# Kernel tuning notes

Hardware: AMD Instinct MI355X
Metric: run time of the kernel (lower is better)

The kernel has to match this reference:

```python
import jax, jax.numpy as jnp
import numpy as np
from jax import lax


def conv2d(x, w, pad):
    return lax.conv_general_dilated(x, w, (1, 1), [(pad, pad), (pad, pad)],
                                    dimension_numbers=('NCHW', 'OIHW', 'NCHW'))


def deform_conv2d(x, offset, w, b, k, pad):
    # torchvision-style DeformConv2d, stride 1, dilation 1, 1 group.
    # offset: [B, 2*k*k, H, W], pairs ordered (dy, dx) per kernel tap (row-major).
    B, C, H, W = x.shape
    KK = k * k
    off = offset.reshape(B, KK, 2, H, W)
    ky, kx = jnp.meshgrid(jnp.arange(k), jnp.arange(k), indexing='ij')
    ky = ky.reshape(1, KK, 1, 1).astype(x.dtype)
    kx = kx.reshape(1, KK, 1, 1).astype(x.dtype)
    gy = jnp.arange(H, dtype=x.dtype).reshape(1, 1, H, 1)
    gx = jnp.arange(W, dtype=x.dtype).reshape(1, 1, 1, W)
    ys = gy + ky - pad + off[:, :, 0]  # [B, KK, H, W]
    xs = gx + kx - pad + off[:, :, 1]
    y0 = jnp.floor(ys)
    x0 = jnp.floor(xs)
    y1 = y0 + 1.0
    x1 = x0 + 1.0
    img = x.reshape(B, C, H * W)

    def corner(yc, xc, wt):
        # zero padding outside the image
        valid = (yc >= 0) & (yc <= H - 1) & (xc >= 0) & (xc <= W - 1)
        idx = (jnp.clip(yc, 0, H - 1) * W + jnp.clip(xc, 0, W - 1)).astype(jnp.int32).reshape(B, -1)
        g = jax.vmap(lambda im, ix: jnp.take(im, ix, axis=1))(img, idx)  # [B, C, KK*H*W]
        return g.reshape(B, C, KK, H, W) * (wt * valid)[:, None]

    v = (corner(y0, x0, (y1 - ys) * (x1 - xs))
         + corner(y0, x1, (y1 - ys) * (xs - x0))
         + corner(y1, x0, (ys - y0) * (x1 - xs))
         + corner(y1, x1, (ys - y0) * (xs - x0)))  # [B, C, KK, H, W]
    out = jnp.einsum('bckhw,ock->bohw', v, w.reshape(w.shape[0], C, KK))
    return out + b[None, :, None, None]


def setup_inputs() -> dict:
    key = jax.random.key(0)
    ks = jax.random.split(key, 16)
    f32 = jnp.float32
    dim = 64

    def rn(k, shape, s):
        return jax.random.normal(k, shape, f32) * s

    return {
        'x': rn(ks[0], (4, dim, 96, 96), 1.0),
        'w_off3': rn(ks[1], (18, dim, 3, 3), 0.01), 'b_off3': jnp.zeros((18,), f32),
        'w_off5': rn(ks[2], (50, dim, 3, 3), 0.01), 'b_off5': jnp.zeros((50,), f32),
        'w_off7': rn(ks[3], (98, dim, 3, 3), 0.01), 'b_off7': jnp.zeros((98,), f32),
        'w_d3': rn(ks[4], (dim, dim, 3, 3), 0.04), 'b_d3': rn(ks[5], (dim,), 0.01),
        'w_d5': rn(ks[6], (dim, dim, 5, 5), 0.025), 'b_d5': rn(ks[7], (dim,), 0.01),
        'w_d7': rn(ks[8], (dim, dim, 7, 7), 0.018), 'b_d7': rn(ks[9], (dim,), 0.01),
        'w_sp': rn(ks[10], (1, 2, 7, 7), 0.1),
        'w_ca1': rn(ks[11], (12, 3 * dim, 1, 1), 0.07),
        'w_ca2': rn(ks[12], (3 * dim, 12, 1, 1), 0.28),
    }


def reference(x, w_off3, b_off3, w_off5, b_off5, w_off7, b_off7,
              w_d3, b_d3, w_d5, b_d5, w_d7, b_d7, w_sp, w_ca1, w_ca2):
    off3 = conv2d(x, w_off3, 1) + b_off3[None, :, None, None]
    off5 = conv2d(x, w_off5, 1) + b_off5[None, :, None, None]
    off7 = conv2d(x, w_off7, 1) + b_off7[None, :, None, None]
    a1 = deform_conv2d(x, off3, w_d3, b_d3, 3, 1)
    a2 = deform_conv2d(x, off5, w_d5, b_d5, 5, 2)
    a3 = deform_conv2d(x, off7, w_d7, b_d7, 7, 3)
    res = jnp.concatenate([a1, a2, a3], axis=1)  # [B, 3C, H, W]

    # SpatialAttention: channel mean/max -> 7x7 conv -> sigmoid
    sp_in = jnp.concatenate([jnp.mean(res, axis=1, keepdims=True),
                             jnp.max(res, axis=1, keepdims=True)], axis=1)
    sp = jax.nn.sigmoid(conv2d(sp_in, w_sp, 3))  # [B, 1, H, W]

    # ChannelAttention: shared MLP on avg- and max-pooled descriptors
    def fc(t):
        return conv2d(jnp.maximum(conv2d(t, w_ca1, 0), 0.0), w_ca2, 0)

    avg = jnp.mean(res, axis=(2, 3), keepdims=True)
    mx = jnp.max(res, axis=(2, 3), keepdims=True)
    ch = jax.nn.sigmoid(fc(avg) + fc(mx))  # [B, 3C, 1, 1]

    C = x.shape[1]
    c1, c2, c3 = ch[:, :C], ch[:, C:2 * C], ch[:, 2 * C:]
    return a1 * (sp + c1) + a2 * (sp + c2) + a3 * (sp + c3)
```

## Files before the change

kernel.cpp:

```cpp
#include <hip/hip_runtime.h>
#include <math.h>

#define H 96
#define W 96
#define HW (H*W)
#define CIN 64
#define NB 4
#define NOFF 166
#define OFFROW 168

typedef __attribute__((ext_vector_type(8)))  short short8;
typedef __attribute__((ext_vector_type(8)))  _Float16 half8;
typedef __attribute__((ext_vector_type(16))) float f32x16;
typedef unsigned short ushort_t;

static const size_t OFF_ALL = 0;
static const size_t RES     = OFF_ALL + (size_t)NB*HW*OFFROW;
static const size_t XB16    = RES + (size_t)NB*192*HW;
static const size_t WTD3    = XB16 + (size_t)NB*64*HW/2;
static const size_t WTD5    = WTD3 + 9*4096/2;
static const size_t WTD7    = WTD5 + 25*4096/2;
static const size_t WOFF    = WTD7 + 49*4096/2;
static const size_t BOFF    = WOFF + 9*192*64/2;
static const size_t SPIN    = BOFF + 192;
static const size_t SPATT   = SPIN + (size_t)NB*2*HW;
static const size_t POOLAVG = SPATT + (size_t)NB*HW;
static const size_t POOLMAX = POOLAVG + NB*192;
static const size_t CHATT   = POOLMAX + NB*192;

__device__ __forceinline__ ushort_t f2h(float f) {
    _Float16 h = (_Float16)f;
    return __builtin_bit_cast(unsigned short, h);
}
__device__ __forceinline__ half8 as_h8(short8 s) {
    return __builtin_bit_cast(half8, s);
}
__device__ __forceinline__ half8 splat8(float f) {
    _Float16 h = (_Float16)f;
    half8 v;
    #pragma unroll
    for (int j = 0; j < 8; j++) v[j] = h;
    return v;
}

__global__ __launch_bounds__(256) void convert_x_nhwc_kernel(const float* __restrict__ x,
                                                             ushort_t* __restrict__ xb) {
    __shared__ ushort_t tile[64][66];
    int t = threadIdx.x;
    int b = blockIdx.x / 144;
    int p0 = (blockIdx.x % 144) * 64;
    int q = t >> 6, ln = t & 63;
    #pragma unroll
    for (int i = 0; i < 16; i++) {
        int c = q * 16 + i;
        tile[ln][c] = f2h(x[((size_t)(b * 64 + c)) * HW + p0 + ln]);
    }
    __syncthreads();
    #pragma unroll
    for (int i = 0; i < 16; i++) {
        int pos = q * 16 + i;
        xb[((size_t)b * HW + p0 + pos) * 64 + ln] = tile[pos][ln];
    }
}

__global__ void convert_wt_all_kernel(const float* __restrict__ w3, const float* __restrict__ w5,
                                      const float* __restrict__ w7,
                                      ushort_t* __restrict__ wt3, ushort_t* __restrict__ wt5,
                                      ushort_t* __restrict__ wt7) {
    int idx = blockIdx.x * 256 + threadIdx.x;
    const float* src; ushort_t* dst; int KK; int o;
    if (idx < 9 * 4096)       { src = w3; dst = wt3; KK = 9;  o = idx; }
    else if (idx < 34 * 4096) { src = w5; dst = wt5; KK = 25; o = idx - 9 * 4096; }
    else if (idx < 83 * 4096) { src = w7; dst = wt7; KK = 49; o = idx - 34 * 4096; }
    else return;
    int j    = o & 7;
    int l31  = (o >> 3) & 31;
    int lh   = (o >> 8) & 1;
    int cs   = (o >> 9) & 3;
    int half = (o >> 11) & 1;
    int kk   = o >> 12;
    int co = half * 32 + l31;
    int c  = cs * 16 + lh * 8 + j;
    dst[o] = f2h(src[((size_t)co * 64 + c) * KK + kk]);
}

__global__ void build_woff_kernel(const float* __restrict__ w3, const float* __restrict__ w5,
                                  const float* __restrict__ w7, const float* __restrict__ b3,
                                  const float* __restrict__ b5, const float* __restrict__ b7,
                                  ushort_t* __restrict__ woff, float* __restrict__ boff) {
    int idx = blockIdx.x * 256 + threadIdx.x;
    if (idx >= 9 * 192 * 64) return;
    int c  = idx & 63;
    int co = (idx >> 6) % 192;
    int kk = idx / (192 * 64);
    float v = 0.f;
    if (co < 18)       v = w3[(co * 64 + c) * 9 + kk];
    else if (co < 68)  v = w5[((co - 18) * 64 + c) * 9 + kk];
    else if (co < 166) v = w7[((co - 68) * 64 + c) * 9 + kk];
    woff[(kk * 192 + co) * 64 + c] = f2h(v);
    if (kk == 0 && c == 0) {
        float bv = 0.f;
        if (co < 18)       bv = b3[co];
        else if (co < 68)  bv = b5[co - 18];
        else if (co < 166) bv = b7[co - 68];
        boff[co] = bv;
    }
}

__global__ __launch_bounds__(256, 3) void offset_mfma_kernel(
    const ushort_t* __restrict__ xb,
    const ushort_t* __restrict__ woff,
    const float* __restrict__ bias_all,
    float* __restrict__ off_all)
{
    __shared__ float red[6144];
    const int t = threadIdx.x;
    const int lane = t & 63, l31 = lane & 31, lh = lane >> 5;
    const int wave = t >> 6;
    const int mhalf = wave >> 1, khalf = wave & 1;
    const int xcd = blockIdx.x & 7, u = blockIdx.x >> 3;
    const int b = xcd >> 1;
    const int v = u * 2 + (xcd & 1);
    const int npos = v * 32 + l31;
    const int h = npos / 96, w = npos % 96;
    const int c0 = 8 * lh;
    const ushort_t* xbase = xb + (size_t)b * HW * 64;

    f32x16 acc0, acc1, acc2;
    #pragma unroll
    for (int r = 0; r < 16; r++) { acc0[r] = 0.f; acc1[r] = 0.f; acc2[r] = 0.f; }

    const int kk0 = khalf ? 5 : 0, kk1 = khalf ? 9 : 5;
    const int mt0 = mhalf * 3;
    for (int kk = kk0; kk < kk1; kk++) {
        int ky = kk / 3, kx = kk % 3;
        int y = h + ky - 1, x = w + kx - 1;
        bool ok = ((unsigned)y < (unsigned)H) && ((unsigned)x < (unsigned)W);
        int o = ok ? (y * W + x) : 0;
        short zm = ok ? (short)0xFFFF : (short)0;
        const ushort_t* px = xbase + (size_t)o * 64 + c0;
        const ushort_t* wk = woff + (size_t)kk * 12288;
        #pragma unroll
        for (int cs = 0; cs < 4; cs++) {
            int cc = cs * 16;
            short8 q = *(const short8*)(px + cc);
            short8 bm;
            #pragma unroll
            for (int j = 0; j < 8; j++) bm[j] = (short)(q[j] & zm);
            half8 bfrag = as_h8(bm);
            half8 a0 = as_h8(*(const short8*)(wk + (size_t)((mt0 + 0) * 32 + l31) * 64 + cc + c0));
            half8 a1 = as_h8(*(const short8*)(wk + (size_t)((mt0 + 1) * 32 + l31) * 64 + cc + c0));
            half8 a2 = as_h8(*(const short8*)(wk + (size_t)((mt0 + 2) * 32 + l31) * 64 + cc + c0));
            acc0 = __builtin_amdgcn_mfma_f32_32x32x16_f16(a0, bfrag, acc0, 0, 0, 0);
            acc1 = __builtin_amdgcn_mfma_f32_32x32x16_f16(a1, bfrag, acc1, 0, 0, 0);
            acc2 = __builtin_amdgcn_mfma_f32_32x32x16_f16(a2, bfrag, acc2, 0, 0, 0);
        }
    }

    if (khalf) {
        float* rp = red + mhalf * 3072;
        #pragma unroll
        for (int r = 0; r < 16; r++) {
            rp[(0 * 16 + r) * 64 + lane] = acc0[r];
            rp[(1 * 16 + r) * 64 + lane] = acc1[r];
            rp[(2 * 16 + r) * 64 + lane] = acc2[r];
        }
    }
    __syncthreads();
    if (!khalf) {
        const float* rp = red + mhalf * 3072;
        #pragma unroll
        for (int r = 0; r < 16; r++) {
            acc0[r] += rp[(0 * 16 + r) * 64 + lane];
            acc1[r] += rp[(1 * 16 + r) * 64 + lane];
            acc2[r] += rp[(2 * 16 + r) * 64 + lane];
        }
        float* row = off_all + ((size_t)b * HW + npos) * OFFROW;
        #pragma unroll
        for (int m = 0; m < 3; m++) {
            const f32x16& a = (m == 0) ? acc0 : (m == 1) ? acc1 : acc2;
            int mt = mt0 + m;
            #pragma unroll
            for (int q = 0; q < 4; q++) {
                int base = mt * 32 + 8 * q + 4 * lh;
                if (base < 166) {
                    float4 vv = make_float4(a[4 * q + 0] + bias_all[base + 0],
                                            a[4 * q + 1] + bias_all[base + 1],
                                            a[4 * q + 2] + bias_all[base + 2],
                                            a[4 * q + 3] + bias_all[base + 3]);
                    *(float4*)(row + base) = vv;
                }
            }
        }
    }
}

__device__ __forceinline__ void store_tile(int b, int tile, int lane, int g,
                                           const float* __restrict__ bias,
                                           const f32x16& acc0, const f32x16& acc1,
                                           float* __restrict__ res)
{
    const int l31 = lane & 31, lh = lane >> 5;
    const int npos = tile * 32 + l31;
    size_t rb = (((size_t)b * 3 + g) * 64) * HW + npos;
    #pragma unroll
    for (int r = 0; r < 16; r++) {
        int co = (r & 3) + 8 * (r >> 2) + 4 * lh;
        res[rb + (size_t)co * HW]        = acc0[r] + bias[co];
        res[rb + (size_t)(co + 32) * HW] = acc1[r] + bias[co + 32];
    }
}

#define MG  5
#define PNY 12
#define PNX 43
#define PXS 144
#define PRS (PNX * PXS)

template<int K, int PAD>
__device__ __forceinline__ void deform_span(
    const float* __restrict__ offp, const ushort_t* __restrict__ wtf,
    int kk0, int kk1, int h, int w, int w0, int l31, int lh,
    const char* lds, f32x16& acc0, f32x16& acc1)
{
    const int lh16 = lh * 16;
    const float2* offp2 = (const float2*)offp;
    float2 off = offp2[kk0];
    for (int kk = kk0; kk < kk1; kk++) {
        float2 noff = offp2[(kk + 1 < kk1) ? kk + 1 : kk];

        int ky = kk / K, kx = kk % K;
        float ys = (float)(h + ky - PAD) + off.x;
        float xs = (float)(w + kx - PAD) + off.y;
        float y0f = floorf(ys), x0f = floorf(xs);
        float fy = ys - y0f, fx = xs - x0f;
        int iy0 = (int)y0f, ix0 = (int)x0f;
        int iy1 = iy0 + 1, ix1 = ix0 + 1;
        float oky0 = ((unsigned)iy0 < (unsigned)H) ? 1.f : 0.f;
        float oky1 = ((unsigned)iy1 < (unsigned)H) ? 1.f : 0.f;
        float okx0 = ((unsigned)ix0 < (unsigned)W) ? 1.f : 0.f;
        float okx1 = ((unsigned)ix1 < (unsigned)W) ? 1.f : 0.f;
        float w00 = (1.f - fy) * (1.f - fx) * oky0 * okx0;
        float w01 = (1.f - fy) * fx * oky0 * okx1;
        float w10 = fy * (1.f - fx) * oky1 * okx0;
        float w11 = fy * fx * oky1 * okx1;
        int cy0 = min(max(iy0, 0), H - 1), cy1 = min(max(iy1, 0), H - 1);
        int cx0 = min(max(ix0, 0), W - 1), cx1 = min(max(ix1, 0), W - 1);
        int r0 = min(max(cy0 - h + MG, 0), PNY - 1);
        int r1 = min(max(cy1 - h + MG, 0), PNY - 1);
        int p0 = min(max(cx0 - w0 + MG, 0), PNX - 1);
        int p1 = min(max(cx1 - w0 + MG, 0), PNX - 1);
        const char* b00 = lds + r0 * PRS + p0 * PXS + lh16;
        const char* b01 = lds + r0 * PRS + p1 * PXS + lh16;
        const char* b10 = lds + r1 * PRS + p0 * PXS + lh16;
        const char* b11 = lds + r1 * PRS + p1 * PXS + lh16;

        half8 W00 = splat8(w00), W01 = splat8(w01);
        half8 W10 = splat8(w10), W11 = splat8(w11);
        const ushort_t* wkf = wtf + (size_t)kk * 4096;
        #pragma unroll
        for (int cs = 0; cs < 4; cs++) {
            half8 q00 = *(const half8*)(b00 + cs * 32);
            half8 q01 = *(const half8*)(b01 + cs * 32);
            half8 q10 = *(const half8*)(b10 + cs * 32);
            half8 q11 = *(const half8*)(b11 + cs * 32);
            half8 bfrag = q00 * W00 + q01 * W01 + q10 * W10 + q11 * W11;
            half8 a0 = as_h8(*(const short8*)(wkf + (size_t)(((0 * 4 + cs) * 2 + lh) * 32 + l31) * 8));
            half8 a1 = as_h8(*(const short8*)(wkf + (size_t)(((1 * 4 + cs) * 2 + lh) * 32 + l31) * 8));
            acc0 = __builtin_amdgcn_mfma_f32_32x32x16_f16(a0, bfrag, acc0, 0, 0, 0);
            acc1 = __builtin_amdgcn_mfma_f32_32x32x16_f16(a1, bfrag, acc1, 0, 0, 0);
        }
        off = noff;
    }
}

__global__ __launch_bounds__(256, 2) void deform_fused_kernel(
    const ushort_t* __restrict__ xb, const float* __restrict__ off_all,
    const ushort_t* __restrict__ wt3, const ushort_t* __restrict__ wt5,
    const ushort_t* __restrict__ wt7,
    const float* __restrict__ b3, const float* __restrict__ b5,
    const float* __restrict__ b7,
    float* __restrict__ res)
{
    __shared__ __align__(16) char lds[PNY * PNX * PXS];
    const int t = threadIdx.x;
    const int wave = t >> 6, lane = t & 63;
    const int xcd = blockIdx.x & 7, u = blockIdx.x >> 3;
    const int b = xcd >> 1;
    const int tile = u * 2 + (xcd & 1);

    const int l31 = lane & 31, lh = lane >> 5;
    const int h  = tile / 3;
    const int w0 = (tile % 3) * 32;
    const int w  = w0 + l31;
    const int npos = h * 96 + w;

    const ushort_t* xsrc = xb + (size_t)b * HW * 64;
    constexpr int NCH = PNY * PNX * 8;
    constexpr int NITER = (NCH + 255) / 256;
    #pragma unroll
    for (int it = 0; it < NITER; it++) {
        int c = t + it * 256;
        if (c < NCH) {
            int rr  = c / (PNX * 8);
            int rem = c - rr * (PNX * 8);
            int pp  = rem >> 3, sub = rem & 7;
            int cy = min(max(h - MG + rr, 0), H - 1);
            int cx = min(max(w0 - MG + pp, 0), W - 1);
            *(float4*)(lds + rr * PRS + pp * PXS + sub * 16) =
                *(const float4*)(xsrc + ((size_t)(cy * W + cx)) * 64 + sub * 8);
        }
    }
    __syncthreads();

    const float* offrow = off_all + ((size_t)b * HW + npos) * OFFROW;

    f32x16 a0A, a1A, a0B, a1B;
    #pragma unroll
    for (int r = 0; r < 16; r++) { a0A[r] = 0.f; a1A[r] = 0.f; a0B[r] = 0.f; a1B[r] = 0.f; }

    if (wave == 0) {
        deform_span<3, 1>(offrow + 0,  wt3, 0, 9,  h, w, w0, l31, lh, lds, a0A, a1A);
        deform_span<5, 2>(offrow + 18, wt5, 0, 12, h, w, w0, l31, lh, lds, a0B, a1B);
    } else if (wave == 1) {
        deform_span<5, 2>(offrow + 18, wt5, 12, 25, h, w, w0, l31, lh, lds, a0A, a1A);
        deform_span<7, 3>(offrow + 68, wt7, 0, 8,   h, w, w0, l31, lh, lds, a0B, a1B);
    } else if (wave == 2) {
        deform_span<7, 3>(offrow + 68, wt7, 8, 29,  h, w, w0, l31, lh, lds, a0A, a1A);
    } else {
        deform_span<7, 3>(offrow + 68, wt7, 29, 49, h, w, w0, l31, lh, lds, a0A, a1A);
    }

    __syncthreads();
    float* slots = (float*)lds;
    if (wave == 1) {
        float* s0 = slots;
        float* s1 = slots + 2048;
        #pragma unroll
        for (int r = 0; r < 16; r++) {
            s0[r * 64 + lane]        = a0A[r];
            s0[(16 + r) * 64 + lane] = a1A[r];
            s1[r * 64 + lane]        = a0B[r];
            s1[(16 + r) * 64 + lane] = a1B[r];
        }
    } else if (wave == 3) {
        float* s2 = slots + 4096;
        #pragma unroll
        for (int r = 0; r < 16; r++) {
            s2[r * 64 + lane]        = a0A[r];
            s2[(16 + r) * 64 + lane] = a1A[r];
        }
    }
    __syncthreads();
    if (wave == 0) {
        store_tile(b, tile, lane, 0, b3, a0A, a1A, res);
        const float* s0 = slots;
        #pragma unroll
        for (int r = 0; r < 16; r++) {
            a0B[r] += s0[r * 64 + lane];
            a1B[r] += s0[(16 + r) * 64 + lane];
        }
        store_tile(b, tile, lane, 1, b5, a0B, a1B, res);
    } else if (wave == 2) {
        const float* s1 = slots + 2048;
        const float* s2 = slots + 4096;
        #pragma unroll
        for (int r = 0; r < 16; r++) {
            a0A[r] += s1[r * 64 + lane] + s2[r * 64 + lane];
            a1A[r] += s1[(16 + r) * 64 + lane] + s2[(16 + r) * 64 + lane];
        }
        store_tile(b, tile, lane, 2, b7, a0A, a1A, res);
    }
}

__global__ void sp_meanmax_kernel(const float* __restrict__ res,
                                  float* __restrict__ spin) {
    int gt  = blockIdx.x * 256 + threadIdx.x;
    int idx = gt >> 2;
    int q   = gt & 3;
    int hw = idx % HW;
    int b  = idx / HW;
    const float* r = res + ((size_t)b * 192 + q * 48) * HW + hw;
    float s = 0.f, m = -3.402823466e+38f;
    for (int c = 0; c < 48; c++) {
        float v = r[(size_t)c * HW];
        s += v;
        m = fmaxf(m, v);
    }
    s += __shfl_xor(s, 1);  m = fmaxf(m, __shfl_xor(m, 1));
    s += __shfl_xor(s, 2);  m = fmaxf(m, __shfl_xor(m, 2));
    if (q == 0) {
        spin[(size_t)b * 2 * HW + hw]      = s * (1.f / 192.f);
        spin[(size_t)b * 2 * HW + HW + hw] = m;
    }
}

__global__ void sp_conv_kernel(const float* __restrict__ spin,
                               const float* __restrict__ w_sp,
                               float* __restrict__ sp) {
    int gt  = blockIdx.x * 256 + threadIdx.x;
    int idx = gt >> 2;
    int q   = gt & 3;
    int w = idx % W;
    int h = (idx / W) % H;
    int b = idx / HW;
    int ci  = q >> 1;
    int dy0 = (q & 1) ? 4 : 0;
    int dy1 = (q & 1) ? 7 : 4;
    const float* pin = spin + ((size_t)b * 2 + ci) * HW;
    const float* wp  = w_sp + ci * 49;
    float acc = 0.f;
    for (int dy = dy0; dy < dy1; dy++) {
        int yy = h + dy - 3;
        if (yy < 0 || yy >= H) continue;
        #pragma unroll
        for (int dx = 0; dx < 7; dx++) {
            int xx = w + dx - 3;
            if (xx < 0 || xx >= W) continue;
            acc = fmaf(pin[yy * W + xx], wp[dy * 7 + dx], acc);
        }
    }
    acc += __shfl_xor(acc, 1);
    acc += __shfl_xor(acc, 2);
    if (q == 0) sp[idx] = 1.f / (1.f + expf(-acc));
}

__global__ void pool_kernel(const float* __restrict__ res,
                            float* __restrict__ avg, float* __restrict__ mx) {
    int bc = blockIdx.x;
    const float* r = res + (size_t)bc * HW;
    int t = threadIdx.x;
    float s = 0.f, m = -3.402823466e+38f;
    for (int i = t; i < HW; i += 256) {
        float v = r[i];
        s += v;
        m = fmaxf(m, v);
    }
    #pragma unroll
    for (int off = 32; off > 0; off >>= 1) {
        s += __shfl_down(s, off);
        m = fmaxf(m, __shfl_down(m, off));
    }
    __shared__ float ss[4], sm[4];
    int wid = t >> 6;
    if ((t & 63) == 0) { ss[wid] = s; sm[wid] = m; }
    __syncthreads();
    if (t == 0) {
        s = ss[0] + ss[1] + ss[2] + ss[3];
        m = fmaxf(fmaxf(sm[0], sm[1]), fmaxf(sm[2], sm[3]));
        avg[bc] = s * (1.f / (float)HW);
        mx[bc]  = m;
    }
}

__global__ void chatt_kernel(const float* __restrict__ avg,
                             const float* __restrict__ mx,
                             const float* __restrict__ w1,
                             const float* __restrict__ w2,
                             float* __restrict__ ch) {
    int b = blockIdx.x;
    int t = threadIdx.x;
    __shared__ float sa[192], sm_[192], h1a[12], h1m[12];
    if (t < 192) { sa[t] = avg[b * 192 + t]; sm_[t] = mx[b * 192 + t]; }
    __syncthreads();
    if (t < 12) {
        float s1 = 0.f, s2 = 0.f;
        for (int c = 0; c < 192; c++) {
            float wv = w1[t * 192 + c];
            s1 = fmaf(wv, sa[c], s1);
            s2 = fmaf(wv, sm_[c], s2);
        }
        h1a[t] = fmaxf(s1, 0.f);
        h1m[t] = fmaxf(s2, 0.f);
    }
    __syncthreads();
    if (t < 192) {
        float s = 0.f;
        #pragma unroll
        for (int j = 0; j < 12; j++)
            s = fmaf(w2[t * 12 + j], h1a[j] + h1m[j], s);
        ch[b * 192 + t] = 1.f / (1.f + expf(-s));
    }
}

__global__ void final_kernel(const float* __restrict__ res,
                             const float* __restrict__ sp,
                             const float* __restrict__ ch,
                             float* __restrict__ out) {
    int idx = blockIdx.x * 256 + threadIdx.x;
    int hw = idx % HW;
    int co = (idx / HW) % 64;
    int b  = idx / (64 * HW);
    size_t rb = (size_t)b * 192 * HW;
    float a1 = res[rb + (size_t)co * HW + hw];
    float a2 = res[rb + (size_t)(64 + co) * HW + hw];
    float a3 = res[rb + (size_t)(128 + co) * HW + hw];
    float spv = sp[(size_t)b * HW + hw];
    float c1 = ch[b * 192 + co];
    float c2 = ch[b * 192 + 64 + co];
    float c3 = ch[b * 192 + 128 + co];
    out[idx] = a1 * (spv + c1) + a2 * (spv + c2) + a3 * (spv + c3);
}

extern "C" void kernel_launch(void* const* d_in, const int* in_sizes, int n_in,
                              void* d_out, int out_size, void* d_ws, size_t ws_size,
                              hipStream_t stream) {
    const float* x      = (const float*)d_in[0];
    const float* w_off3 = (const float*)d_in[1];
    const float* b_off3 = (const float*)d_in[2];
    const float* w_off5 = (const float*)d_in[3];
    const float* b_off5 = (const float*)d_in[4];
    const float* w_off7 = (const float*)d_in[5];
    const float* b_off7 = (const float*)d_in[6];
    const float* w_d3   = (const float*)d_in[7];
    const float* b_d3   = (const float*)d_in[8];
    const float* w_d5   = (const float*)d_in[9];
    const float* b_d5   = (const float*)d_in[10];
    const float* w_d7   = (const float*)d_in[11];
    const float* b_d7   = (const float*)d_in[12];
    const float* w_sp   = (const float*)d_in[13];
    const float* w_ca1  = (const float*)d_in[14];
    const float* w_ca2  = (const float*)d_in[15];

    float* ws = (float*)d_ws;
    float* off_all = ws + OFF_ALL;
    float* res     = ws + RES;
    ushort_t* xb16 = (ushort_t*)(ws + XB16);
    ushort_t* wt3  = (ushort_t*)(ws + WTD3);
    ushort_t* wt5  = (ushort_t*)(ws + WTD5);
    ushort_t* wt7  = (ushort_t*)(ws + WTD7);
    ushort_t* woff = (ushort_t*)(ws + WOFF);
    float* boff = ws + BOFF;
    float* spin = ws + SPIN;
    float* sp   = ws + SPATT;
    float* avgp = ws + POOLAVG;
    float* mxp  = ws + POOLMAX;
    float* chp  = ws + CHATT;

    convert_x_nhwc_kernel<<<576, 256, 0, stream>>>(x, xb16);
    convert_wt_all_kernel<<<1328, 256, 0, stream>>>(w_d3, w_d5, w_d7, wt3, wt5, wt7);
    build_woff_kernel<<<432, 256, 0, stream>>>(w_off3, w_off5, w_off7,
                                               b_off3, b_off5, b_off7, woff, boff);

    offset_mfma_kernel<<<1152, 256, 0, stream>>>(xb16, woff, boff, off_all);

    deform_fused_kernel<<<1152, 256, 0, stream>>>(xb16, off_all, wt3, wt5, wt7,
                                                  b_d3, b_d5, b_d7, res);

    sp_meanmax_kernel<<<576, 256, 0, stream>>>(res, spin);
    sp_conv_kernel<<<576, 256, 0, stream>>>(spin, w_sp, sp);
    pool_kernel<<<768, 256, 0, stream>>>(res, avgp, mxp);
    chatt_kernel<<<4, 256, 0, stream>>>(avgp, mxp, w_ca1, w_ca2, chp);

    final_kernel<<<9216, 256, 0, stream>>>(res, sp, chp, (float*)d_out);
}
```

Measured before the change: 163.0 us.

## Prefetch deform weight fragments, merge weight-prep kernels, parallelize channel-attention MLP

The deformable-conv inner loop now loads the next kernel tap's eight weight fragments into registers one iteration ahead, so global weight-load latency overlaps the bilinear sampling and MFMA work. The two weight-conversion kernels are merged into one launch to save a kernel launch. The channel-attention first layer is spread over 192 threads with a shuffle reduction instead of 12 serial threads. The prefetch adds register pressure in a kernel that already targets two blocks per SM, which could cost occupancy or cause spills.

```diff
diff --git a/kernel.cpp b/kernel.cpp
--- a/kernel.cpp
+++ b/kernel.cpp
@@ -63,46 +63,47 @@
     }
 }
 
-__global__ void convert_wt_all_kernel(const float* __restrict__ w3, const float* __restrict__ w5,
-                                      const float* __restrict__ w7,
-                                      ushort_t* __restrict__ wt3, ushort_t* __restrict__ wt5,
-                                      ushort_t* __restrict__ wt7) {
+__global__ void convert_weights_kernel(const float* __restrict__ w3, const float* __restrict__ w5,
+                                       const float* __restrict__ w7,
+                                       const float* __restrict__ ob3, const float* __restrict__ ob5,
+                                       const float* __restrict__ ob7,
+                                       const float* __restrict__ ow3, const float* __restrict__ ow5,
+                                       const float* __restrict__ ow7,
+                                       ushort_t* __restrict__ wt3, ushort_t* __restrict__ wt5,
+                                       ushort_t* __restrict__ wt7,
+                                       ushort_t* __restrict__ woff, float* __restrict__ boff) {
     int idx = blockIdx.x * 256 + threadIdx.x;
-    const float* src; ushort_t* dst; int KK; int o;
-    if (idx < 9 * 4096)       { src = w3; dst = wt3; KK = 9;  o = idx; }
-    else if (idx < 34 * 4096) { src = w5; dst = wt5; KK = 25; o = idx - 9 * 4096; }
-    else if (idx < 83 * 4096) { src = w7; dst = wt7; KK = 49; o = idx - 34 * 4096; }
-    else return;
-    int j    = o & 7;
-    int l31  = (o >> 3) & 31;
-    int lh   = (o >> 8) & 1;
-    int cs   = (o >> 9) & 3;
-    int half = (o >> 11) & 1;
-    int kk   = o >> 12;
-    int co = half * 32 + l31;
-    int c  = cs * 16 + lh * 8 + j;
-    dst[o] = f2h(src[((size_t)co * 64 + c) * KK + kk]);
-}
-
-__global__ void build_woff_kernel(const float* __restrict__ w3, const float* __restrict__ w5,
-                                  const float* __restrict__ w7, const float* __restrict__ b3,
-                                  const float* __restrict__ b5, const float* __restrict__ b7,
-                                  ushort_t* __restrict__ woff, float* __restrict__ boff) {
-    int idx = blockIdx.x * 256 + threadIdx.x;
-    if (idx >= 9 * 192 * 64) return;
-    int c  = idx & 63;
-    int co = (idx >> 6) % 192;
-    int kk = idx / (192 * 64);
+    if (idx < 83 * 4096) {
+        const float* src; ushort_t* dst; int KK; int o;
+        if (idx < 9 * 4096)       { src = w3; dst = wt3; KK = 9;  o = idx; }
+        else if (idx < 34 * 4096) { src = w5; dst = wt5; KK = 25; o = idx - 9 * 4096; }
+        else                      { src = w7; dst = wt7; KK = 49; o = idx - 34 * 4096; }
+        int j    = o & 7;
+        int l31  = (o >> 3) & 31;
+        int lh   = (o >> 8) & 1;
+        int cs   = (o >> 9) & 3;
+        int half = (o >> 11) & 1;
+        int kk   = o >> 12;
+        int co = half * 32 + l31;
+        int c  = cs * 16 + lh * 8 + j;
+        dst[o] = f2h(src[((size_t)co * 64 + c) * KK + kk]);
+        return;
+    }
+    int o = idx - 83 * 4096;
+    if (o >= 9 * 192 * 64) return;
+    int c  = o & 63;
+    int co = (o >> 6) % 192;
+    int kk = o / (192 * 64);
     float v = 0.f;
-    if (co < 18)       v = w3[(co * 64 + c) * 9 + kk];
-    else if (co < 68)  v = w5[((co - 18) * 64 + c) * 9 + kk];
-    else if (co < 166) v = w7[((co - 68) * 64 + c) * 9 + kk];
+    if (co < 18)       v = ow3[(co * 64 + c) * 9 + kk];
+    else if (co < 68)  v = ow5[((co - 18) * 64 + c) * 9 + kk];
+    else if (co < 166) v = ow7[((co - 68) * 64 + c) * 9 + kk];
     woff[(kk * 192 + co) * 64 + c] = f2h(v);
     if (kk == 0 && c == 0) {
         float bv = 0.f;
-        if (co < 18)       bv = b3[co];
-        else if (co < 68)  bv = b5[co - 18];
-        else if (co < 166) bv = b7[co - 68];
+        if (co < 18)       bv = ob3[co];
+        else if (co < 68)  bv = ob5[co - 18];
+        else if (co < 166) bv = ob7[co - 68];
         boff[co] = bv;
     }
 }
@@ -225,9 +226,34 @@
 {
     const int lh16 = lh * 16;
     const float2* offp2 = (const float2*)offp;
+    const ushort_t* wbase = wtf + ((size_t)(lh * 32 + l31)) * 8;
+
     float2 off = offp2[kk0];
+    short8 wc0, wc1, wc2, wc3, wc4, wc5, wc6, wc7;
+    {
+        const ushort_t* wk = wbase + (size_t)kk0 * 4096;
+        wc0 = *(const short8*)(wk + 0 * 512);
+        wc1 = *(const short8*)(wk + 1 * 512);
+        wc2 = *(const short8*)(wk + 2 * 512);
+        wc3 = *(const short8*)(wk + 3 * 512);
+        wc4 = *(const short8*)(wk + 2048 + 0 * 512);
+        wc5 = *(const short8*)(wk + 2048 + 1 * 512);
+        wc6 = *(const short8*)(wk + 2048 + 2 * 512);
+        wc7 = *(const short8*)(wk + 2048 + 3 * 512);
+    }
+
     for (int kk = kk0; kk < kk1; kk++) {
-        float2 noff = offp2[(kk + 1 < kk1) ? kk + 1 : kk];
+        int kn = (kk + 1 < kk1) ? (kk + 1) : kk;
+        float2 noff = offp2[kn];
+        const ushort_t* wkn = wbase + (size_t)kn * 4096;
+        short8 wn0 = *(const short8*)(wkn + 0 * 512);
+        short8 wn1 = *(const short8*)(wkn + 1 * 512);
+        short8 wn2 = *(const short8*)(wkn + 2 * 512);
+        short8 wn3 = *(const short8*)(wkn + 3 * 512);
+        short8 wn4 = *(const short8*)(wkn + 2048 + 0 * 512);
+        short8 wn5 = *(const short8*)(wkn + 2048 + 1 * 512);
+        short8 wn6 = *(const short8*)(wkn + 2048 + 2 * 512);
+        short8 wn7 = *(const short8*)(wkn + 2048 + 3 * 512);
 
         int ky = kk / K, kx = kk % K;
         float ys = (float)(h + ky - PAD) + off.x;
@@ -257,7 +283,6 @@
 
         half8 W00 = splat8(w00), W01 = splat8(w01);
         half8 W10 = splat8(w10), W11 = splat8(w11);
-        const ushort_t* wkf = wtf + (size_t)kk * 4096;
         #pragma unroll
         for (int cs = 0; cs < 4; cs++) {
             half8 q00 = *(const half8*)(b00 + cs * 32);
@@ -265,12 +290,14 @@
             half8 q10 = *(const half8*)(b10 + cs * 32);
             half8 q11 = *(const half8*)(b11 + cs * 32);
             half8 bfrag = q00 * W00 + q01 * W01 + q10 * W10 + q11 * W11;
-            half8 a0 = as_h8(*(const short8*)(wkf + (size_t)(((0 * 4 + cs) * 2 + lh) * 32 + l31) * 8));
-            half8 a1 = as_h8(*(const short8*)(wkf + (size_t)(((1 * 4 + cs) * 2 + lh) * 32 + l31) * 8));
-            acc0 = __builtin_amdgcn_mfma_f32_32x32x16_f16(a0, bfrag, acc0, 0, 0, 0);
-            acc1 = __builtin_amdgcn_mfma_f32_32x32x16_f16(a1, bfrag, acc1, 0, 0, 0);
+            short8 a0s = (cs == 0) ? wc0 : (cs == 1) ? wc1 : (cs == 2) ? wc2 : wc3;
+            short8 a1s = (cs == 0) ? wc4 : (cs == 1) ? wc5 : (cs == 2) ? wc6 : wc7;
+            acc0 = __builtin_amdgcn_mfma_f32_32x32x16_f16(as_h8(a0s), bfrag, acc0, 0, 0, 0);
+            acc1 = __builtin_amdgcn_mfma_f32_32x32x16_f16(as_h8(a1s), bfrag, acc1, 0, 0, 0);
         }
         off = noff;
+        wc0 = wn0; wc1 = wn1; wc2 = wn2; wc3 = wn3;
+        wc4 = wn4; wc5 = wn5; wc6 = wn6; wc7 = wn7;
     }
 }
 
@@ -463,15 +490,25 @@
     __shared__ float sa[192], sm_[192], h1a[12], h1m[12];
     if (t < 192) { sa[t] = avg[b * 192 + t]; sm_[t] = mx[b * 192 + t]; }
     __syncthreads();
-    if (t < 12) {
+    if (t < 192) {
+        int j = t >> 4, lg = t & 15;
         float s1 = 0.f, s2 = 0.f;
-        for (int c = 0; c < 192; c++) {
-            float wv = w1[t * 192 + c];
+        #pragma unroll
+        for (int i = 0; i < 12; i++) {
+            int c = lg + i * 16;
+            float wv = w1[j * 192 + c];
             s1 = fmaf(wv, sa[c], s1);
             s2 = fmaf(wv, sm_[c], s2);
         }
-        h1a[t] = fmaxf(s1, 0.f);
-        h1m[t] = fmaxf(s2, 0.f);
+        #pragma unroll
+        for (int d = 1; d < 16; d <<= 1) {
+            s1 += __shfl_xor(s1, d);
+            s2 += __shfl_xor(s2, d);
+        }
+        if (lg == 0) {
+            h1a[j] = fmaxf(s1, 0.f);
+            h1m[j] = fmaxf(s2, 0.f);
+        }
     }
     __syncthreads();
     if (t < 192) {
@@ -538,9 +575,10 @@
     float* chp  = ws + CHATT;
 
     convert_x_nhwc_kernel<<<576, 256, 0, stream>>>(x, xb16);
-    convert_wt_all_kernel<<<1328, 256, 0, stream>>>(w_d3, w_d5, w_d7, wt3, wt5, wt7);
-    build_woff_kernel<<<432, 256, 0, stream>>>(w_off3, w_off5, w_off7,
-                                               b_off3, b_off5, b_off7, woff, boff);
+    convert_weights_kernel<<<1760, 256, 0, stream>>>(w_d3, w_d5, w_d7,
+                                                     b_off3, b_off5, b_off7,
+                                                     w_off3, w_off5, w_off7,
+                                                     wt3, wt5, wt7, woff, boff);
 
     offset_mfma_kernel<<<1152, 256, 0, stream>>>(xb16, woff, boff, off_all);
 
```

Result: no change. 163.5 us (+0.3%).
